# Optimization experiments

Hardware: AMD Instinct MI355X
Metric: run time of the kernel (lower is better)

The kernel has to match this reference:

```python
import jax, jax.numpy as jnp
import numpy as np
from jax import lax

H1, H2, H3, T, IN = 15, 60, 20, 15, 1


def lstm_layer(x, W_ih, W_hh, b_ih, b_hh):
    # x: [B, T, in] -> hs: [B, T, H]; PyTorch gate order i, f, g, o
    B = x.shape[0]
    H = W_hh.shape[1]
    h0 = jnp.zeros((B, H), x.dtype)
    c0 = jnp.zeros((B, H), x.dtype)
    b = b_ih + b_hh

    def step(carry, xt):
        h, c = carry
        g = xt @ W_ih.T + h @ W_hh.T + b  # [B, 4H]
        i, f, gg, o = jnp.split(g, 4, axis=-1)
        i = jax.nn.sigmoid(i)
        f = jax.nn.sigmoid(f)
        gg = jnp.tanh(gg)
        o = jax.nn.sigmoid(o)
        c = f * c + i * gg
        h = o * jnp.tanh(c)
        return (h, c), h

    _, hs = lax.scan(step, (h0, c0), jnp.swapaxes(x, 0, 1))  # hs: [T, B, H]
    return jnp.swapaxes(hs, 0, 1)


def setup_inputs() -> dict:
    key = jax.random.key(0)
    ks = jax.random.split(key, 16)
    s = 0.1
    B = 131072
    inp = {
        "x": jax.random.normal(ks[0], (B, T, IN), jnp.float32),
        "W_ih0": jax.random.normal(ks[1], (4 * H1, IN), jnp.float32) * s,
        "W_hh0": jax.random.normal(ks[2], (4 * H1, H1), jnp.float32) * s,
        "b_ih0": jax.random.normal(ks[3], (4 * H1,), jnp.float32) * s,
        "b_hh0": jax.random.normal(ks[4], (4 * H1,), jnp.float32) * s,
        "W_ih1": jax.random.normal(ks[5], (4 * H1, H1), jnp.float32) * s,
        "W_hh1": jax.random.normal(ks[6], (4 * H1, H1), jnp.float32) * s,
        "b_ih1": jax.random.normal(ks[7], (4 * H1,), jnp.float32) * s,
        "b_hh1": jax.random.normal(ks[8], (4 * H1,), jnp.float32) * s,
        "W1": jax.random.normal(ks[9], (H2, H1), jnp.float32) * s,
        "b1": jax.random.normal(ks[10], (H2,), jnp.float32) * s,
        "W2": jax.random.normal(ks[11], (H3, H2), jnp.float32) * s,
        "b2": jax.random.normal(ks[12], (H3,), jnp.float32) * s,
        "W3": jax.random.normal(ks[13], (1, H3), jnp.float32) * s,
        "b3": jax.random.normal(ks[14], (1,), jnp.float32) * s,
    }
    return inp


def reference(x, W_ih0, W_hh0, b_ih0, b_hh0, W_ih1, W_hh1, b_ih1, b_hh1, W1, b1, W2, b2, W3, b3):
    h1 = lstm_layer(x, W_ih0, W_hh0, b_ih0, b_hh0)   # [B, T, H1]
    h2 = lstm_layer(h1, W_ih1, W_hh1, b_ih1, b_hh1)  # [B, T, H1] (eval mode: no dropout)
    feat = h2[:, :, -1]                              # [B, T] == [B, 15]
    out1 = feat @ W1.T + b1                          # [B, 60]
    out2 = out1 @ W2.T + b2                          # [B, 20]
    out = out2 @ W3.T + b3                           # [B, 1]
    return out
```

## Files before the change

### kernel.cpp

```cpp
#include <hip/hip_runtime.h>

#define HH   15
#define TT   15
#define NH2  60
#define NH3  20

#define LOG2E 1.44269504088896340736f
#define L2E2  2.88539008177792680736f

typedef _Float16 f16x8 __attribute__((ext_vector_type(8)));
typedef float    f32x4 __attribute__((ext_vector_type(4)));

#define WS_V  2048
#define WS_CB 2063

__device__ __forceinline__ float fast_rcp(float x)  { return __builtin_amdgcn_rcpf(x); }
__device__ __forceinline__ float fast_exp2(float x) { return __builtin_amdgcn_exp2f(x); }

__global__ void lstm_prep(const float* __restrict__ Wih0, const float* __restrict__ Whh0,
                          const float* __restrict__ bih0, const float* __restrict__ bhh0,
                          const float* __restrict__ Wih1, const float* __restrict__ Whh1,
                          const float* __restrict__ bih1, const float* __restrict__ bhh1,
                          const float* __restrict__ W1, const float* __restrict__ b1,
                          const float* __restrict__ W2, const float* __restrict__ b2,
                          const float* __restrict__ W3, const float* __restrict__ b3,
                          float* __restrict__ wsf)
{
    const int tid = threadIdx.x;
    unsigned* wsu = (unsigned*)wsf;

    {
        const int f = tid >> 6, l = tid & 63;
        const int n = f & 3;
        const bool isL2 = (f >= 4);
        const int u = l & 15, g = l >> 4;
        const float sc = (n == 2) ? L2E2 : LOG2E;
        const int r = n * 15 + (u < 15 ? u : 0);
        float vals[8];
        #pragma unroll
        for (int j = 0; j < 8; ++j) {
            const int k = g * 8 + j;
            float v = 0.0f;
            if (u < 15) {
                if (!isL2) {
                    if (k < 15)       v = Whh0[r * 15 + k];
                    else if (k == 15) v = Wih0[r];
                    else if (k == 16) v = bih0[r] + bhh0[r];
                } else {
                    if (k < 15)       v = Wih1[r * 15 + k];
                    else if (k == 15) v = bih1[r] + bhh1[r];
                    else if (k < 31)  v = Whh1[r * 15 + (k - 16)];
                }
            }
            vals[j] = v * sc;
        }
        #pragma unroll
        for (int d = 0; d < 4; ++d) {
            union { _Float16 h[2]; unsigned u32; } p;
            p.h[0] = (_Float16)vals[2 * d];
            p.h[1] = (_Float16)vals[2 * d + 1];
            wsu[f * 256 + l * 4 + d] = p.u32;
        }
    }

    __shared__ float sU[NH2];
    if (tid < NH2) {
        float ua = 0.0f;
        #pragma unroll
        for (int k = 0; k < NH3; ++k) ua = fmaf(W3[k], W2[k * NH2 + tid], ua);
        sU[tid] = ua;
    }
    __syncthreads();
    if (tid < TT) {
        float v = 0.0f;
        for (int j = 0; j < NH2; ++j) v = fmaf(sU[j], W1[j * HH + tid], v);
        wsf[WS_V + tid] = v;
    }
    if (tid == 0) {
        float c = b3[0];
        for (int k = 0; k < NH3; ++k) c = fmaf(W3[k], b2[k], c);
        for (int j = 0; j < NH2; ++j) c = fmaf(sU[j], b1[j], c);
        wsf[WS_CB] = c;
    }
}

__global__ __launch_bounds__(256)
void lstm_mfma(const float* __restrict__ x, const float* __restrict__ wsf,
               float* __restrict__ out, int B)
{
    __shared__ __align__(16) _Float16 lds[4][2][2][16][40];

    const int tid = threadIdx.x;
    const int wid = tid >> 6;
    const int l   = tid & 63;
    const int u   = l & 15;
    const int g   = l >> 4;
    const int wbase = (blockIdx.x * 4 + wid) * 32;

    {
        unsigned* zw = (unsigned*)&lds[wid][0][0][0][0];
        #pragma unroll
        for (int i = 0; i < 20; ++i) zw[l + 64 * i] = 0u;
    }

    const uint4* wsq = (const uint4*)wsf;
    union FU { uint4 q; f16x8 h; };
#define LOADB(name, fidx) f16x8 name; { FU t_; t_.q = wsq[(fidx) * 64 + l]; name = t_.h; }
    LOADB(B0, 0) LOADB(B1, 1) LOADB(B2, 2) LOADB(B3, 3)
    LOADB(B4, 4) LOADB(B5, 5) LOADB(B6, 6) LOADB(B7, 7)
#undef LOADB

    if (l < 16) {
        lds[wid][0][0][l][16] = (_Float16)1.0f;
        lds[wid][0][1][l][15] = (_Float16)1.0f;
        lds[wid][1][0][l][16] = (_Float16)1.0f;
        lds[wid][1][1][l][15] = (_Float16)1.0f;
    }

    const int u1col = (u == 15) ? 31 : u;

    const float cb = wsf[WS_CB];
    f32x4 accA = {cb, cb, cb, cb}, accB = accA;
    f32x4 c1A = {0.f,0.f,0.f,0.f}, c2A = c1A, c1B = c1A, c2B = c1A;
    const f32x4 zc = {0.f,0.f,0.f,0.f};

    const int til = (l >> 4) & 1;
    const float* xp = x + (size_t)(wbase + (l & 31)) * TT;

#define MFMA(a, b, c) __builtin_amdgcn_mfma_f32_16x16x32_f16((a), (b), (c), 0, 0, 0)

#define UPDC(i, d0, d1, d2, d3, Cst) \
        const float ei = fast_exp2(-d0[i]); \
        const float ef = fast_exp2(-d1[i]); \
        const float eg = fast_exp2(d2[i]); \
        const float eo = fast_exp2(-d3[i]); \
        const float dn1 = (1.0f + ei) * (eg + 1.0f); \
        const float dn2 = 1.0f + ef; \
        const float t1 = fmaf(L2E2, eg, -L2E2); \
        const float r  = fast_rcp(dn1 * dn2); \
        const float cc = fmaf(Cst[i], dn1, t1 * dn2) * r; \
        Cst[i] = cc; \
        const float ec = fast_exp2(cc); \
        const float hh = (ec - 1.0f) * fast_rcp((1.0f + eo) * (ec + 1.0f));

#define UPD1(i, T, Cst, d0, d1, d2, d3) { \
        UPDC(i, d0, d1, d2, d3, Cst) \
        const _Float16 hf = (_Float16)hh; \
        lds[wid][T][0][4 * g + (i)][u] = hf; \
        lds[wid][T][1][4 * g + (i)][u1col] = hf; }

#define UPD2(i, T, Cst, Acc, e0, e1, e2, e3) { \
        UPDC(i, e0, e1, e2, e3, Cst) \
        lds[wid][T][1][4 * g + (i)][16 + u] = (_Float16)hh; \
        Acc[i] = fmaf(hh, vt, Acc[i]); }

    {
        const float x0 = xp[0];
        if (l < 32) lds[wid][til][0][u][15] = (_Float16)x0;
    }
    f16x8 a1A = *(const f16x8*)&lds[wid][0][0][u][g * 8];
    f16x8 a1B = *(const f16x8*)&lds[wid][1][0][u][g * 8];
    f32x4 dA0 = MFMA(a1A, B0, zc), dA1 = MFMA(a1A, B1, zc);
    f32x4 dA2 = MFMA(a1A, B2, zc), dA3 = MFMA(a1A, B3, zc);
    f32x4 dB0 = MFMA(a1B, B0, zc), dB1 = MFMA(a1B, B1, zc);
    f32x4 dB2 = MFMA(a1B, B2, zc), dB3 = MFMA(a1B, B3, zc);

    #pragma unroll 2
    for (int t = 0; t < TT - 1; ++t) {
        const float xn = xp[t + 1];

        UPD1(0, 0, c1A, dA0, dA1, dA2, dA3) UPD1(1, 0, c1A, dA0, dA1, dA2, dA3)
        UPD1(2, 0, c1A, dA0, dA1, dA2, dA3) UPD1(3, 0, c1A, dA0, dA1, dA2, dA3)
        UPD1(0, 1, c1B, dB0, dB1, dB2, dB3) UPD1(1, 1, c1B, dB0, dB1, dB2, dB3)
        UPD1(2, 1, c1B, dB0, dB1, dB2, dB3) UPD1(3, 1, c1B, dB0, dB1, dB2, dB3)

        const f16x8 a2A = *(const f16x8*)&lds[wid][0][1][u][g * 8];
        f32x4 eA0 = MFMA(a2A, B4, zc), eA1 = MFMA(a2A, B5, zc);
        f32x4 eA2 = MFMA(a2A, B6, zc), eA3 = MFMA(a2A, B7, zc);
        const f16x8 a2B = *(const f16x8*)&lds[wid][1][1][u][g * 8];
        f32x4 eB0 = MFMA(a2B, B4, zc), eB1 = MFMA(a2B, B5, zc);
        f32x4 eB2 = MFMA(a2B, B6, zc), eB3 = MFMA(a2B, B7, zc);

        if (l < 32) lds[wid][til][0][u][15] = (_Float16)xn;
        a1A = *(const f16x8*)&lds[wid][0][0][u][g * 8];
        dA0 = MFMA(a1A, B0, zc); dA1 = MFMA(a1A, B1, zc);
        dA2 = MFMA(a1A, B2, zc); dA3 = MFMA(a1A, B3, zc);
        a1B = *(const f16x8*)&lds[wid][1][0][u][g * 8];
        dB0 = MFMA(a1B, B0, zc); dB1 = MFMA(a1B, B1, zc);
        dB2 = MFMA(a1B, B2, zc); dB3 = MFMA(a1B, B3, zc);

        const float vt = wsf[WS_V + t];
        UPD2(0, 0, c2A, accA, eA0, eA1, eA2, eA3) UPD2(1, 0, c2A, accA, eA0, eA1, eA2, eA3)
        UPD2(2, 0, c2A, accA, eA0, eA1, eA2, eA3) UPD2(3, 0, c2A, accA, eA0, eA1, eA2, eA3)
        UPD2(0, 1, c2B, accB, eB0, eB1, eB2, eB3) UPD2(1, 1, c2B, accB, eB0, eB1, eB2, eB3)
        UPD2(2, 1, c2B, accB, eB0, eB1, eB2, eB3) UPD2(3, 1, c2B, accB, eB0, eB1, eB2, eB3)
    }

    {
        UPD1(0, 0, c1A, dA0, dA1, dA2, dA3) UPD1(1, 0, c1A, dA0, dA1, dA2, dA3)
        UPD1(2, 0, c1A, dA0, dA1, dA2, dA3) UPD1(3, 0, c1A, dA0, dA1, dA2, dA3)
        UPD1(0, 1, c1B, dB0, dB1, dB2, dB3) UPD1(1, 1, c1B, dB0, dB1, dB2, dB3)
        UPD1(2, 1, c1B, dB0, dB1, dB2, dB3) UPD1(3, 1, c1B, dB0, dB1, dB2, dB3)

        const f16x8 a2A = *(const f16x8*)&lds[wid][0][1][u][g * 8];
        f32x4 eA0 = MFMA(a2A, B4, zc), eA1 = MFMA(a2A, B5, zc);
        f32x4 eA2 = MFMA(a2A, B6, zc), eA3 = MFMA(a2A, B7, zc);
        const f16x8 a2B = *(const f16x8*)&lds[wid][1][1][u][g * 8];
        f32x4 eB0 = MFMA(a2B, B4, zc), eB1 = MFMA(a2B, B5, zc);
        f32x4 eB2 = MFMA(a2B, B6, zc), eB3 = MFMA(a2B, B7, zc);

        const float vt = wsf[WS_V + (TT - 1)];
        UPD2(0, 0, c2A, accA, eA0, eA1, eA2, eA3) UPD2(1, 0, c2A, accA, eA0, eA1, eA2, eA3)
        UPD2(2, 0, c2A, accA, eA0, eA1, eA2, eA3) UPD2(3, 0, c2A, accA, eA0, eA1, eA2, eA3)
        UPD2(0, 1, c2B, accB, eB0, eB1, eB2, eB3) UPD2(1, 1, c2B, accB, eB0, eB1, eB2, eB3)
        UPD2(2, 1, c2B, accB, eB0, eB1, eB2, eB3) UPD2(3, 1, c2B, accB, eB0, eB1, eB2, eB3)
    }
#undef UPD1
#undef UPD2
#undef UPDC
#undef MFMA

    if (u == 14) {
        out[wbase + 4 * g + 0] = accA[0];
        out[wbase + 4 * g + 1] = accA[1];
        out[wbase + 4 * g + 2] = accA[2];
        out[wbase + 4 * g + 3] = accA[3];
        out[wbase + 16 + 4 * g + 0] = accB[0];
        out[wbase + 16 + 4 * g + 1] = accB[1];
        out[wbase + 16 + 4 * g + 2] = accB[2];
        out[wbase + 16 + 4 * g + 3] = accB[3];
    }
}

extern "C" void kernel_launch(void* const* d_in, const int* in_sizes, int n_in,
                              void* d_out, int out_size, void* d_ws, size_t ws_size,
                              hipStream_t stream) {
    (void)n_in; (void)ws_size; (void)out_size;
    const float* x    = (const float*)d_in[0];
    const float* Wih0 = (const float*)d_in[1];
    const float* Whh0 = (const float*)d_in[2];
    const float* bih0 = (const float*)d_in[3];
    const float* bhh0 = (const float*)d_in[4];
    const float* Wih1 = (const float*)d_in[5];
    const float* Whh1 = (const float*)d_in[6];
    const float* bih1 = (const float*)d_in[7];
    const float* bhh1 = (const float*)d_in[8];
    const float* W1   = (const float*)d_in[9];
    const float* b1   = (const float*)d_in[10];
    const float* W2   = (const float*)d_in[11];
    const float* b2   = (const float*)d_in[12];
    const float* W3   = (const float*)d_in[13];
    const float* b3   = (const float*)d_in[14];
    float* out = (float*)d_out;
    float* wsf = (float*)d_ws;

    const int B = in_sizes[0] / TT;

    lstm_prep<<<1, 512, 0, stream>>>(Wih0, Whh0, bih0, bhh0,
                                     Wih1, Whh1, bih1, bhh1,
                                     W1, b1, W2, b2, W3, b3, wsf);

    const int grid = B / (32 * 4);
    lstm_mfma<<<grid, 256, 0, stream>>>(x, wsf, out, B);
}
```

Before: 143.1 us.

## Share one LDS A-tile between both LSTM layers and drop duplicate stores

Merges the two per-layer LDS activation tiles into one row layout: [h1(0..14), x, 1, h2(17..31)]. The layer-2 weights are repacked to match, so a single A-fragment load feeds both the layer-1 and layer-2 MFMAs. This halves LDS footprint, removes the duplicated h1 store and one of the two fragment reads per step, and skips the final h2 store. In exchange, the layer-1 and layer-2 MFMAs now share one read, so the x/h1 writes must complete before it, which tightens dependencies and may reduce overlap.

After: 144.2 us. Within noise of the previous version (+0.8%).

```diff
diff --git a/kernel.cpp b/kernel.cpp
--- a/kernel.cpp
+++ b/kernel.cpp
@@ -48,8 +48,8 @@
                     else if (k == 16) v = bih0[r] + bhh0[r];
                 } else {
                     if (k < 15)       v = Wih1[r * 15 + k];
-                    else if (k == 15) v = bih1[r] + bhh1[r];
-                    else if (k < 31)  v = Whh1[r * 15 + (k - 16)];
+                    else if (k == 16) v = bih1[r] + bhh1[r];
+                    else if (k >= 17) v = Whh1[r * 15 + (k - 17)];
                 }
             }
             vals[j] = v * sc;
@@ -88,7 +88,7 @@
 void lstm_mfma(const float* __restrict__ x, const float* __restrict__ wsf,
                float* __restrict__ out, int B)
 {
-    __shared__ __align__(16) _Float16 lds[4][2][2][16][40];
+    __shared__ __align__(16) _Float16 lds[4][2][16][40];
 
     const int tid = threadIdx.x;
     const int wid = tid >> 6;
@@ -98,9 +98,9 @@
     const int wbase = (blockIdx.x * 4 + wid) * 32;
 
     {
-        unsigned* zw = (unsigned*)&lds[wid][0][0][0][0];
-        #pragma unroll
-        for (int i = 0; i < 20; ++i) zw[l + 64 * i] = 0u;
+        unsigned* zw = (unsigned*)&lds[wid][0][0][0];
+        #pragma unroll
+        for (int i = 0; i < 10; ++i) zw[l + 64 * i] = 0u;
     }
 
     const uint4* wsq = (const uint4*)wsf;
@@ -110,22 +110,18 @@
     LOADB(B4, 4) LOADB(B5, 5) LOADB(B6, 6) LOADB(B7, 7)
 #undef LOADB
 
-    if (l < 16) {
-        lds[wid][0][0][l][16] = (_Float16)1.0f;
-        lds[wid][0][1][l][15] = (_Float16)1.0f;
-        lds[wid][1][0][l][16] = (_Float16)1.0f;
-        lds[wid][1][1][l][15] = (_Float16)1.0f;
-    }
-
-    const int u1col = (u == 15) ? 31 : u;
+    const int til = (l >> 4) & 1;
+    const float* xp = x + (size_t)(wbase + (l & 31)) * TT;
+
+    if (l < 32) {
+        lds[wid][til][u][16] = (_Float16)1.0f;
+        lds[wid][til][u][15] = (_Float16)xp[0];
+    }
 
     const float cb = wsf[WS_CB];
     f32x4 accA = {cb, cb, cb, cb}, accB = accA;
     f32x4 c1A = {0.f,0.f,0.f,0.f}, c2A = c1A, c1B = c1A, c2B = c1A;
     const f32x4 zc = {0.f,0.f,0.f,0.f};
-
-    const int til = (l >> 4) & 1;
-    const float* xp = x + (size_t)(wbase + (l & 31)) * TT;
 
 #define MFMA(a, b, c) __builtin_amdgcn_mfma_f32_16x16x32_f16((a), (b), (c), 0, 0, 0)
 
@@ -145,25 +141,23 @@
 
 #define UPD1(i, T, Cst, d0, d1, d2, d3) { \
         UPDC(i, d0, d1, d2, d3, Cst) \
-        const _Float16 hf = (_Float16)hh; \
-        lds[wid][T][0][4 * g + (i)][u] = hf; \
-        lds[wid][T][1][4 * g + (i)][u1col] = hf; }
+        lds[wid][T][4 * g + (i)][u] = (_Float16)hh; }
 
 #define UPD2(i, T, Cst, Acc, e0, e1, e2, e3) { \
         UPDC(i, e0, e1, e2, e3, Cst) \
-        lds[wid][T][1][4 * g + (i)][16 + u] = (_Float16)hh; \
+        lds[wid][T][4 * g + (i)][17 + u] = (_Float16)hh; \
         Acc[i] = fmaf(hh, vt, Acc[i]); }
 
-    {
-        const float x0 = xp[0];
-        if (l < 32) lds[wid][til][0][u][15] = (_Float16)x0;
-    }
-    f16x8 a1A = *(const f16x8*)&lds[wid][0][0][u][g * 8];
-    f16x8 a1B = *(const f16x8*)&lds[wid][1][0][u][g * 8];
-    f32x4 dA0 = MFMA(a1A, B0, zc), dA1 = MFMA(a1A, B1, zc);
-    f32x4 dA2 = MFMA(a1A, B2, zc), dA3 = MFMA(a1A, B3, zc);
-    f32x4 dB0 = MFMA(a1B, B0, zc), dB1 = MFMA(a1B, B1, zc);
-    f32x4 dB2 = MFMA(a1B, B2, zc), dB3 = MFMA(a1B, B3, zc);
+#define UPD2L(i, T, Cst, Acc, e0, e1, e2, e3) { \
+        UPDC(i, e0, e1, e2, e3, Cst) \
+        Acc[i] = fmaf(hh, vt, Acc[i]); }
+
+    f16x8 aA = *(const f16x8*)&lds[wid][0][u][g * 8];
+    f16x8 aB = *(const f16x8*)&lds[wid][1][u][g * 8];
+    f32x4 dA0 = MFMA(aA, B0, zc), dA1 = MFMA(aA, B1, zc);
+    f32x4 dA2 = MFMA(aA, B2, zc), dA3 = MFMA(aA, B3, zc);
+    f32x4 dB0 = MFMA(aB, B0, zc), dB1 = MFMA(aB, B1, zc);
+    f32x4 dB2 = MFMA(aB, B2, zc), dB3 = MFMA(aB, B3, zc);
 
     #pragma unroll 2
     for (int t = 0; t < TT - 1; ++t) {
@@ -174,20 +168,19 @@
         UPD1(0, 1, c1B, dB0, dB1, dB2, dB3) UPD1(1, 1, c1B, dB0, dB1, dB2, dB3)
         UPD1(2, 1, c1B, dB0, dB1, dB2, dB3) UPD1(3, 1, c1B, dB0, dB1, dB2, dB3)
 
-        const f16x8 a2A = *(const f16x8*)&lds[wid][0][1][u][g * 8];
-        f32x4 eA0 = MFMA(a2A, B4, zc), eA1 = MFMA(a2A, B5, zc);
-        f32x4 eA2 = MFMA(a2A, B6, zc), eA3 = MFMA(a2A, B7, zc);
-        const f16x8 a2B = *(const f16x8*)&lds[wid][1][1][u][g * 8];
-        f32x4 eB0 = MFMA(a2B, B4, zc), eB1 = MFMA(a2B, B5, zc);
-        f32x4 eB2 = MFMA(a2B, B6, zc), eB3 = MFMA(a2B, B7, zc);
-
-        if (l < 32) lds[wid][til][0][u][15] = (_Float16)xn;
-        a1A = *(const f16x8*)&lds[wid][0][0][u][g * 8];
-        dA0 = MFMA(a1A, B0, zc); dA1 = MFMA(a1A, B1, zc);
-        dA2 = MFMA(a1A, B2, zc); dA3 = MFMA(a1A, B3, zc);
-        a1B = *(const f16x8*)&lds[wid][1][0][u][g * 8];
-        dB0 = MFMA(a1B, B0, zc); dB1 = MFMA(a1B, B1, zc);
-        dB2 = MFMA(a1B, B2, zc); dB3 = MFMA(a1B, B3, zc);
+        if (l < 32) lds[wid][til][u][15] = (_Float16)xn;
+
+        aA = *(const f16x8*)&lds[wid][0][u][g * 8];
+        aB = *(const f16x8*)&lds[wid][1][u][g * 8];
+
+        f32x4 eA0 = MFMA(aA, B4, zc), eA1 = MFMA(aA, B5, zc);
+        f32x4 eA2 = MFMA(aA, B6, zc), eA3 = MFMA(aA, B7, zc);
+        f32x4 eB0 = MFMA(aB, B4, zc), eB1 = MFMA(aB, B5, zc);
+        f32x4 eB2 = MFMA(aB, B6, zc), eB3 = MFMA(aB, B7, zc);
+        dA0 = MFMA(aA, B0, zc); dA1 = MFMA(aA, B1, zc);
+        dA2 = MFMA(aA, B2, zc); dA3 = MFMA(aA, B3, zc);
+        dB0 = MFMA(aB, B0, zc); dB1 = MFMA(aB, B1, zc);
+        dB2 = MFMA(aB, B2, zc); dB3 = MFMA(aB, B3, zc);
 
         const float vt = wsf[WS_V + t];
         UPD2(0, 0, c2A, accA, eA0, eA1, eA2, eA3) UPD2(1, 0, c2A, accA, eA0, eA1, eA2, eA3)
@@ -202,21 +195,22 @@
         UPD1(0, 1, c1B, dB0, dB1, dB2, dB3) UPD1(1, 1, c1B, dB0, dB1, dB2, dB3)
         UPD1(2, 1, c1B, dB0, dB1, dB2, dB3) UPD1(3, 1, c1B, dB0, dB1, dB2, dB3)
 
-        const f16x8 a2A = *(const f16x8*)&lds[wid][0][1][u][g * 8];
-        f32x4 eA0 = MFMA(a2A, B4, zc), eA1 = MFMA(a2A, B5, zc);
-        f32x4 eA2 = MFMA(a2A, B6, zc), eA3 = MFMA(a2A, B7, zc);
-        const f16x8 a2B = *(const f16x8*)&lds[wid][1][1][u][g * 8];
-        f32x4 eB0 = MFMA(a2B, B4, zc), eB1 = MFMA(a2B, B5, zc);
-        f32x4 eB2 = MFMA(a2B, B6, zc), eB3 = MFMA(a2B, B7, zc);
+        aA = *(const f16x8*)&lds[wid][0][u][g * 8];
+        aB = *(const f16x8*)&lds[wid][1][u][g * 8];
+        f32x4 eA0 = MFMA(aA, B4, zc), eA1 = MFMA(aA, B5, zc);
+        f32x4 eA2 = MFMA(aA, B6, zc), eA3 = MFMA(aA, B7, zc);
+        f32x4 eB0 = MFMA(aB, B4, zc), eB1 = MFMA(aB, B5, zc);
+        f32x4 eB2 = MFMA(aB, B6, zc), eB3 = MFMA(aB, B7, zc);
 
         const float vt = wsf[WS_V + (TT - 1)];
-        UPD2(0, 0, c2A, accA, eA0, eA1, eA2, eA3) UPD2(1, 0, c2A, accA, eA0, eA1, eA2, eA3)
-        UPD2(2, 0, c2A, accA, eA0, eA1, eA2, eA3) UPD2(3, 0, c2A, accA, eA0, eA1, eA2, eA3)
-        UPD2(0, 1, c2B, accB, eB0, eB1, eB2, eB3) UPD2(1, 1, c2B, accB, eB0, eB1, eB2, eB3)
-        UPD2(2, 1, c2B, accB, eB0, eB1, eB2, eB3) UPD2(3, 1, c2B, accB, eB0, eB1, eB2, eB3)
+        UPD2L(0, 0, c2A, accA, eA0, eA1, eA2, eA3) UPD2L(1, 0, c2A, accA, eA0, eA1, eA2, eA3)
+        UPD2L(2, 0, c2A, accA, eA0, eA1, eA2, eA3) UPD2L(3, 0, c2A, accA, eA0, eA1, eA2, eA3)
+        UPD2L(0, 1, c2B, accB, eB0, eB1, eB2, eB3) UPD2L(1, 1, c2B, accB, eB0, eB1, eB2, eB3)
+        UPD2L(2, 1, c2B, accB, eB0, eB1, eB2, eB3) UPD2L(3, 1, c2B, accB, eB0, eB1, eB2, eB3)
     }
 #undef UPD1
 #undef UPD2
+#undef UPD2L
 #undef UPDC
 #undef MFMA
 
```
